# Kernel tuning notes

Measured on AMD Instinct MI355X. Metric: run time of the kernel, lower is better.

## Reference

```python
import jax, jax.numpy as jnp
import numpy as np

EPS = 1e-08

def setup_inputs() -> dict:
    key = jax.random.key(0)
    ks = jax.random.split(key, 5)
    B, T, D, L = 8, 4096, 1024, 24
    data = jax.random.normal(ks[0], (B, T, D), dtype=jnp.float32)
    W_enc = jax.random.normal(ks[1], (L, D), dtype=jnp.float32) * (1.0 / np.sqrt(D))
    b_enc = jax.random.normal(ks[2], (L,), dtype=jnp.float32) * 0.01
    W_dec = jax.random.normal(ks[3], (D, L), dtype=jnp.float32) * (1.0 / np.sqrt(L))
    b_dec = jax.random.normal(ks[4], (D,), dtype=jnp.float32) * 0.01
    ecs = jnp.array([0.1], dtype=jnp.float32)  # error_correction_strength
    ep = jnp.array([1.0], dtype=jnp.float32)   # energy_preservation
    return {"data": data, "W_enc": W_enc, "b_enc": b_enc,
            "W_dec": W_dec, "b_dec": b_dec,
            "error_correction_strength": ecs, "energy_preservation": ep}

def _l2(x):
    return jnp.linalg.norm(x, axis=-1, keepdims=True)

def reference(data, W_enc, b_enc, W_dec, b_dec, error_correction_strength, energy_preservation):
    ecs = error_correction_strength[0]
    ep = energy_preservation[0]
    # --- encode_to_lattice ---
    in_e = _l2(data)                                   # [B,T,1]
    proj = jnp.einsum('btd,ld->btl', data, W_enc) + b_enc
    lattice_points = jnp.round(proj / ecs) * ecs       # quantize to lattice grid
    out_e = _l2(lattice_points)
    lattice = lattice_points * (in_e / (out_e + EPS)) * ep
    # --- decode_from_lattice ---
    in_e2 = _l2(lattice)
    corrected = jnp.where(jnp.abs(lattice) > ecs, lattice, 0.0)
    res = jnp.einsum('btl,dl->btd', corrected, W_dec) + b_dec
    out_e2 = _l2(res)
    return res * (in_e2 / (out_e2 + EPS)) * ep
```

## Files before the change

kernel.cpp:

```cpp
#include <hip/hip_runtime.h>
#include <math.h>

#define EPS 1e-8f

typedef float vfloat4 __attribute__((ext_vector_type(4)));

__global__ void prep_all(const float* __restrict__ W_enc,
                         const float* __restrict__ Wd, const float* __restrict__ bd,
                         float* __restrict__ wt, float* __restrict__ G,
                         float* __restrict__ h, float* __restrict__ bb) {
    int b = blockIdx.x;
    int lane = threadIdx.x;
    if (b < 384) {
        int i = b * 64 + lane;
        int k = i / 24, l = i - k * 24;
        wt[i] = W_enc[l * 1024 + k];
        return;
    }
    b -= 384;
    float s = 0.f;
    if (b < 576) {
        int l = b / 24, m = b - (b / 24) * 24;
        for (int d = lane; d < 1024; d += 64) s = fmaf(Wd[d * 24 + l], Wd[d * 24 + m], s);
    } else if (b < 600) {
        int l = b - 576;
        for (int d = lane; d < 1024; d += 64) s = fmaf(Wd[d * 24 + l], bd[d], s);
    } else {
        for (int d = lane; d < 1024; d += 64) s = fmaf(bd[d], bd[d], s);
    }
    for (int off = 32; off; off >>= 1) s += __shfl_down(s, off);
    if (lane == 0) {
        if (b < 576) G[b] = s;
        else if (b < 600) h[b - 576] = s;
        else *bb = s;
    }
}


constexpr int BROWS   = 128;
constexpr int LD_TILE = 32;
constexpr int TILE_F  = BROWS * LD_TILE;
constexpr int NW      = 8;
constexpr int SMEM_F  = NW * TILE_F;

__global__ __launch_bounds__(512, 2)
void leech_main(const float* __restrict__ data,
                const float* __restrict__ b_enc,
                const float* __restrict__ Wd,
                const float* __restrict__ b_dec,
                const float* __restrict__ ecs_p,
                const float* __restrict__ ep_p,
                const float* __restrict__ wt,
                const float* __restrict__ G,
                const float* __restrict__ h,
                const float* __restrict__ bbp,
                float* __restrict__ out)
{
    __shared__ float smem[SMEM_F];
    const int tid = threadIdx.x;
    const int w = tid >> 6;
    const int r = tid & 63;
    const int rowbase = blockIdx.x * BROWS;

    float* tile = smem + w * TILE_F;

    const int lrow = r >> 3;
    const int lk   = (r & 7) * 4;
    const int rb   = r & 31;

    float proj0[24], proj1[24];
#pragma unroll
    for (int l = 0; l < 24; ++l) { proj0[l] = 0.f; proj1[l] = 0.f; }
    float ssq0 = 0.f, ssq1 = 0.f;

    const int kw = __builtin_amdgcn_readfirstlane((tid >> 6) * 128);

    float4 buf[16];
#pragma unroll
    for (int it = 0; it < 16; ++it)
        buf[it] = *reinterpret_cast<const float4*>(
            data + (size_t)(rowbase + it * 8 + lrow) * 1024 + kw + lk);

    for (int sc = 0; sc < 4; ++sc) {
#pragma unroll
        for (int it = 0; it < 16; ++it) {
            const int row = it * 8 + lrow;
            const int rbw = row & 31;
            float* t = tile + row * LD_TILE;
            t[(lk + 0) ^ rbw] = buf[it].x;
            t[(lk + 1) ^ rbw] = buf[it].y;
            t[(lk + 2) ^ rbw] = buf[it].z;
            t[(lk + 3) ^ rbw] = buf[it].w;
        }
        if (sc < 3) {
            const int k0n = kw + (sc + 1) * 32;
#pragma unroll
            for (int it = 0; it < 16; ++it)
                buf[it] = *reinterpret_cast<const float4*>(
                    data + (size_t)(rowbase + it * 8 + lrow) * 1024 + k0n + lk);
        }
        const float* x0 = tile + r * LD_TILE;
        const float* x1 = tile + (r + 64) * LD_TILE;
        const int kofs = __builtin_amdgcn_readfirstlane(kw + sc * 32);
#pragma unroll 4
        for (int kk = 0; kk < 32; ++kk) {
            const float a = x0[kk ^ rb];
            const float b = x1[kk ^ rb];
            ssq0 = fmaf(a, a, ssq0);
            ssq1 = fmaf(b, b, ssq1);
            const float* wp = wt + (size_t)(kofs + kk) * 24;
#pragma unroll
            for (int l = 0; l < 24; ++l) {
                const float wv = wp[l];
                proj0[l] = fmaf(wv, a, proj0[l]);
                proj1[l] = fmaf(wv, b, proj1[l]);
            }
        }
    }

#pragma unroll
    for (int l = 0; l < 24; ++l) {
        smem[w * TILE_F + l * 64 + r]        = proj0[l];
        smem[w * TILE_F + (24 + l) * 64 + r] = proj1[l];
    }
    smem[w * TILE_F + 48 * 64 + r] = ssq0;
    smem[w * TILE_F + 49 * 64 + r] = ssq1;
    __syncthreads();

    float p0[24], p1[24];
#pragma unroll
    for (int l = 0; l < 24; ++l) {
        float a0 = smem[0 * TILE_F + l * 64 + r] + smem[1 * TILE_F + l * 64 + r];
        float a1 = smem[2 * TILE_F + l * 64 + r] + smem[3 * TILE_F + l * 64 + r];
        float a2 = smem[4 * TILE_F + l * 64 + r] + smem[5 * TILE_F + l * 64 + r];
        float a3 = smem[6 * TILE_F + l * 64 + r] + smem[7 * TILE_F + l * 64 + r];
        p0[l] = (a0 + a1) + (a2 + a3);
        float b0 = smem[0 * TILE_F + (24 + l) * 64 + r] + smem[1 * TILE_F + (24 + l) * 64 + r];
        float b1 = smem[2 * TILE_F + (24 + l) * 64 + r] + smem[3 * TILE_F + (24 + l) * 64 + r];
        float b2 = smem[4 * TILE_F + (24 + l) * 64 + r] + smem[5 * TILE_F + (24 + l) * 64 + r];
        float b3 = smem[6 * TILE_F + (24 + l) * 64 + r] + smem[7 * TILE_F + (24 + l) * 64 + r];
        p1[l] = (b0 + b1) + (b2 + b3);
    }
    float ss0, ss1;
    {
        float a0 = smem[0 * TILE_F + 48 * 64 + r] + smem[1 * TILE_F + 48 * 64 + r];
        float a1 = smem[2 * TILE_F + 48 * 64 + r] + smem[3 * TILE_F + 48 * 64 + r];
        float a2 = smem[4 * TILE_F + 48 * 64 + r] + smem[5 * TILE_F + 48 * 64 + r];
        float a3 = smem[6 * TILE_F + 48 * 64 + r] + smem[7 * TILE_F + 48 * 64 + r];
        ss0 = (a0 + a1) + (a2 + a3);
        float b0 = smem[0 * TILE_F + 49 * 64 + r] + smem[1 * TILE_F + 49 * 64 + r];
        float b1 = smem[2 * TILE_F + 49 * 64 + r] + smem[3 * TILE_F + 49 * 64 + r];
        float b2 = smem[4 * TILE_F + 49 * 64 + r] + smem[5 * TILE_F + 49 * 64 + r];
        float b3 = smem[6 * TILE_F + 49 * 64 + r] + smem[7 * TILE_F + 49 * 64 + r];
        ss1 = (b0 + b1) + (b2 + b3);
    }
    __syncthreads();

    const float ecs = ecs_p[0];
    const float ep  = ep_p[0];

    float c0[24], c1[24];
    float s2a, s2b;
    {
        const float in_e = sqrtf(ss0);
        float lp[24]; float oe = 0.f;
#pragma unroll
        for (int l = 0; l < 24; ++l) {
            const float pp = p0[l] + b_enc[l];
            const float q = rintf(pp / ecs) * ecs;
            lp[l] = q;
            oe = fmaf(q, q, oe);
        }
        const float s1 = in_e / (sqrtf(oe) + EPS) * ep;
        float ie = 0.f;
#pragma unroll
        for (int l = 0; l < 24; ++l) {
            const float lat = lp[l] * s1;
            ie = fmaf(lat, lat, ie);
            c0[l] = (fabsf(lat) > ecs) ? lat : 0.f;
        }
        const float in_e2 = sqrtf(ie);
        float qacc = bbp[0];
#pragma unroll
        for (int l = 0; l < 24; ++l) {
            float s = 2.f * h[l];
#pragma unroll
            for (int m = 0; m < 24; ++m)
                s = fmaf(G[l * 24 + m], c0[m], s);
            qacc = fmaf(s, c0[l], qacc);
        }
        const float out_e2 = sqrtf(fmaxf(qacc, 0.f));
        s2a = in_e2 / (out_e2 + EPS) * ep;
    }
    {
        const float in_e = sqrtf(ss1);
        float lp[24]; float oe = 0.f;
#pragma unroll
        for (int l = 0; l < 24; ++l) {
            const float pp = p1[l] + b_enc[l];
            const float q = rintf(pp / ecs) * ecs;
            lp[l] = q;
            oe = fmaf(q, q, oe);
        }
        const float s1 = in_e / (sqrtf(oe) + EPS) * ep;
        float ie = 0.f;
#pragma unroll
        for (int l = 0; l < 24; ++l) {
            const float lat = lp[l] * s1;
            ie = fmaf(lat, lat, ie);
            c1[l] = (fabsf(lat) > ecs) ? lat : 0.f;
        }
        const float in_e2 = sqrtf(ie);
        float qacc = bbp[0];
#pragma unroll
        for (int l = 0; l < 24; ++l) {
            float s = 2.f * h[l];
#pragma unroll
            for (int m = 0; m < 24; ++m)
                s = fmaf(G[l * 24 + m], c1[m], s);
            qacc = fmaf(s, c1[l], qacc);
        }
        const float out_e2 = sqrtf(fmaxf(qacc, 0.f));
        s2b = in_e2 / (out_e2 + EPS) * ep;
    }

    for (int sc = 0; sc < 4; ++sc) {
        const int d0 = __builtin_amdgcn_readfirstlane(kw + sc * 32);
        float* t0 = tile + r * LD_TILE;
        float* t1 = tile + (r + 64) * LD_TILE;
#pragma unroll 4
        for (int dd = 0; dd < 32; ++dd) {
            const int d = d0 + dd;
            const float* wr = Wd + d * 24;
            const float bv = b_dec[d];
            float acc0 = bv, acc1 = bv;
#pragma unroll
            for (int l = 0; l < 24; ++l) {
                const float wv = wr[l];
                acc0 = fmaf(wv, c0[l], acc0);
                acc1 = fmaf(wv, c1[l], acc1);
            }
            t0[dd ^ rb] = acc0 * s2a;
            t1[dd ^ rb] = acc1 * s2b;
        }
#pragma unroll
        for (int it = 0; it < 16; ++it) {
            const int row = it * 8 + lrow;
            const int rbw = row & 31;
            const float* t = tile + row * LD_TILE;
            vfloat4 v;
            v.x = t[(lk + 0) ^ rbw];
            v.y = t[(lk + 1) ^ rbw];
            v.z = t[(lk + 2) ^ rbw];
            v.w = t[(lk + 3) ^ rbw];
            __builtin_nontemporal_store(v, reinterpret_cast<vfloat4*>(
                out + (size_t)(rowbase + row) * 1024 + d0 + lk));
        }
    }
}


extern "C" void kernel_launch(void* const* d_in, const int* in_sizes, int n_in,
                              void* d_out, int out_size, void* d_ws, size_t ws_size,
                              hipStream_t stream) {
    const float* data  = (const float*)d_in[0];
    const float* W_enc = (const float*)d_in[1];
    const float* b_enc = (const float*)d_in[2];
    const float* W_dec = (const float*)d_in[3];
    const float* b_dec = (const float*)d_in[4];
    const float* ecs   = (const float*)d_in[5];
    const float* ep    = (const float*)d_in[6];
    float* out = (float*)d_out;

    float* ws = (float*)d_ws;
    float* wt = ws;
    float* G  = ws + 24576;
    float* h  = ws + 25152;
    float* bb = ws + 25176;

    const int rows = in_sizes[0] / 1024;

    hipLaunchKernelGGL(prep_all, dim3(985), dim3(64), 0, stream,
                       W_enc, W_dec, b_dec, wt, G, h, bb);
    hipLaunchKernelGGL(leech_main, dim3(rows / BROWS), dim3(512), 0, stream,
                       data, b_enc, W_dec, b_dec, ecs, ep, wt, G, h, bb, out);
}
```

Measured before the change: 312.6 us.

## Load data rows directly into registers and stage weights per-wave in LDS

Removes the swizzled LDS transpose tile for input and output. Each thread now loads its two rows' 32-float chunks straight into vector registers and writes decoder results with direct per-row float4 nontemporal stores. Encoder and decoder weight slices are staged per wave into a small LDS region and read back as float4 broadcasts, with loads for the next chunk issued ahead of compute. The cross-wave reduction buffer now packs both rows as float2. The cost is that lanes access memory 4 KB apart, which may reduce global coalescing efficiency and raise register pressure.

```diff
diff --git a/kernel.cpp b/kernel.cpp
--- a/kernel.cpp
+++ b/kernel.cpp
@@ -4,6 +4,7 @@
 #define EPS 1e-8f
 
 typedef float vfloat4 __attribute__((ext_vector_type(4)));
+typedef float vfloat2 __attribute__((ext_vector_type(2)));
 
 __global__ void prep_all(const float* __restrict__ W_enc,
                          const float* __restrict__ Wd, const float* __restrict__ bd,
@@ -37,11 +38,11 @@
 }
 
 
-constexpr int BROWS   = 128;
-constexpr int LD_TILE = 32;
-constexpr int TILE_F  = BROWS * LD_TILE;
-constexpr int NW      = 8;
-constexpr int SMEM_F  = NW * TILE_F;
+constexpr int BROWS  = 128;
+constexpr int NW     = 8;
+constexpr int WREG_F = 800;
+constexpr int COMB_F = 25 * 64 * 2;
+constexpr int SMEM_F = NW * WREG_F + NW * COMB_F;
 
 __global__ __launch_bounds__(512, 2)
 void leech_main(const float* __restrict__ data,
@@ -62,97 +63,100 @@
     const int r = tid & 63;
     const int rowbase = blockIdx.x * BROWS;
 
-    float* tile = smem + w * TILE_F;
-
-    const int lrow = r >> 3;
-    const int lk   = (r & 7) * 4;
-    const int rb   = r & 31;
+    float* wreg = smem + w * WREG_F;
+    vfloat2* cw = (vfloat2*)(smem + NW * WREG_F) + w * 25 * 64;
+    vfloat2* cb = (vfloat2*)(smem + NW * WREG_F);
+
+    const int kw = __builtin_amdgcn_readfirstlane((tid >> 6) * 128);
+
+    const size_t row0 = (size_t)(rowbase + r);
+    const size_t row1 = row0 + 64;
+    const float* pr0 = data + row0 * 1024 + kw;
+    const float* pr1 = data + row1 * 1024 + kw;
 
     float proj0[24], proj1[24];
 #pragma unroll
     for (int l = 0; l < 24; ++l) { proj0[l] = 0.f; proj1[l] = 0.f; }
     float ssq0 = 0.f, ssq1 = 0.f;
 
-    const int kw = __builtin_amdgcn_readfirstlane((tid >> 6) * 128);
-
-    float4 buf[16];
-#pragma unroll
-    for (int it = 0; it < 16; ++it)
-        buf[it] = *reinterpret_cast<const float4*>(
-            data + (size_t)(rowbase + it * 8 + lrow) * 1024 + kw + lk);
-
-    for (int sc = 0; sc < 4; ++sc) {
-#pragma unroll
-        for (int it = 0; it < 16; ++it) {
-            const int row = it * 8 + lrow;
-            const int rbw = row & 31;
-            float* t = tile + row * LD_TILE;
-            t[(lk + 0) ^ rbw] = buf[it].x;
-            t[(lk + 1) ^ rbw] = buf[it].y;
-            t[(lk + 2) ^ rbw] = buf[it].z;
-            t[(lk + 3) ^ rbw] = buf[it].w;
-        }
-        if (sc < 3) {
-            const int k0n = kw + (sc + 1) * 32;
-#pragma unroll
-            for (int it = 0; it < 16; ++it)
-                buf[it] = *reinterpret_cast<const float4*>(
-                    data + (size_t)(rowbase + it * 8 + lrow) * 1024 + k0n + lk);
-        }
-        const float* x0 = tile + r * LD_TILE;
-        const float* x1 = tile + (r + 64) * LD_TILE;
-        const int kofs = __builtin_amdgcn_readfirstlane(kw + sc * 32);
-#pragma unroll 4
-        for (int kk = 0; kk < 32; ++kk) {
-            const float a = x0[kk ^ rb];
-            const float b = x1[kk ^ rb];
-            ssq0 = fmaf(a, a, ssq0);
-            ssq1 = fmaf(b, b, ssq1);
-            const float* wp = wt + (size_t)(kofs + kk) * 24;
-#pragma unroll
-            for (int l = 0; l < 24; ++l) {
-                const float wv = wp[l];
-                proj0[l] = fmaf(wv, a, proj0[l]);
-                proj1[l] = fmaf(wv, b, proj1[l]);
-            }
-        }
-    }
+    vfloat4 xa0[8], xa1[8], xb0[8], xb1[8];
+    vfloat4 ew0, ew1, ew2;
+
+#define XLOAD(X0, X1, sc) { \
+    _Pragma("unroll") \
+    for (int g = 0; g < 8; ++g) { \
+        X0[g] = *(const vfloat4*)(pr0 + (sc) * 32 + g * 4); \
+        X1[g] = *(const vfloat4*)(pr1 + (sc) * 32 + g * 4); \
+    } }
+
+#define EWLOAD(sc) { \
+    const float* gs_ = wt + (size_t)(kw + (sc) * 32) * 24 + r * 12; \
+    ew0 = *(const vfloat4*)gs_; \
+    ew1 = *(const vfloat4*)(gs_ + 4); \
+    ew2 = *(const vfloat4*)(gs_ + 8); }
+
+#define EWSTORE() { \
+    float* d_ = wreg + r * 12; \
+    *(vfloat4*)d_ = ew0; *(vfloat4*)(d_ + 4) = ew1; *(vfloat4*)(d_ + 8) = ew2; }
+
+#define ENC_COMP(X0, X1) { \
+    _Pragma("unroll") \
+    for (int kk = 0; kk < 32; ++kk) { \
+        const float a = X0[kk >> 2][kk & 3]; \
+        const float b = X1[kk >> 2][kk & 3]; \
+        ssq0 = fmaf(a, a, ssq0); \
+        ssq1 = fmaf(b, b, ssq1); \
+        const float* wr_ = wreg + kk * 24; \
+        vfloat4 q[6]; \
+        _Pragma("unroll") \
+        for (int t = 0; t < 6; ++t) q[t] = *(const vfloat4*)(wr_ + t * 4); \
+        _Pragma("unroll") \
+        for (int l = 0; l < 24; ++l) { \
+            const float wv = q[l >> 2][l & 3]; \
+            proj0[l] = fmaf(wv, a, proj0[l]); \
+            proj1[l] = fmaf(wv, b, proj1[l]); \
+        } \
+    } }
+
+    EWLOAD(0); XLOAD(xa0, xa1, 0); EWSTORE();
+    XLOAD(xb0, xb1, 1); EWLOAD(1);
+    ENC_COMP(xa0, xa1);
+    EWSTORE(); EWLOAD(2); XLOAD(xa0, xa1, 2);
+    ENC_COMP(xb0, xb1);
+    EWSTORE(); EWLOAD(3); XLOAD(xb0, xb1, 3);
+    ENC_COMP(xa0, xa1);
+    EWSTORE();
+    ENC_COMP(xb0, xb1);
 
 #pragma unroll
     for (int l = 0; l < 24; ++l) {
-        smem[w * TILE_F + l * 64 + r]        = proj0[l];
-        smem[w * TILE_F + (24 + l) * 64 + r] = proj1[l];
-    }
-    smem[w * TILE_F + 48 * 64 + r] = ssq0;
-    smem[w * TILE_F + 49 * 64 + r] = ssq1;
+        vfloat2 v; v.x = proj0[l]; v.y = proj1[l];
+        cw[l * 64 + r] = v;
+    }
+    {
+        vfloat2 v; v.x = ssq0; v.y = ssq1;
+        cw[24 * 64 + r] = v;
+    }
     __syncthreads();
 
     float p0[24], p1[24];
 #pragma unroll
     for (int l = 0; l < 24; ++l) {
-        float a0 = smem[0 * TILE_F + l * 64 + r] + smem[1 * TILE_F + l * 64 + r];
-        float a1 = smem[2 * TILE_F + l * 64 + r] + smem[3 * TILE_F + l * 64 + r];
-        float a2 = smem[4 * TILE_F + l * 64 + r] + smem[5 * TILE_F + l * 64 + r];
-        float a3 = smem[6 * TILE_F + l * 64 + r] + smem[7 * TILE_F + l * 64 + r];
-        p0[l] = (a0 + a1) + (a2 + a3);
-        float b0 = smem[0 * TILE_F + (24 + l) * 64 + r] + smem[1 * TILE_F + (24 + l) * 64 + r];
-        float b1 = smem[2 * TILE_F + (24 + l) * 64 + r] + smem[3 * TILE_F + (24 + l) * 64 + r];
-        float b2 = smem[4 * TILE_F + (24 + l) * 64 + r] + smem[5 * TILE_F + (24 + l) * 64 + r];
-        float b3 = smem[6 * TILE_F + (24 + l) * 64 + r] + smem[7 * TILE_F + (24 + l) * 64 + r];
-        p1[l] = (b0 + b1) + (b2 + b3);
+        vfloat2 a0 = cb[(0 * 25 + l) * 64 + r] + cb[(1 * 25 + l) * 64 + r];
+        vfloat2 a1 = cb[(2 * 25 + l) * 64 + r] + cb[(3 * 25 + l) * 64 + r];
+        vfloat2 a2 = cb[(4 * 25 + l) * 64 + r] + cb[(5 * 25 + l) * 64 + r];
+        vfloat2 a3 = cb[(6 * 25 + l) * 64 + r] + cb[(7 * 25 + l) * 64 + r];
+        vfloat2 s = (a0 + a1) + (a2 + a3);
+        p0[l] = s.x; p1[l] = s.y;
     }
     float ss0, ss1;
     {
-        float a0 = smem[0 * TILE_F + 48 * 64 + r] + smem[1 * TILE_F + 48 * 64 + r];
-        float a1 = smem[2 * TILE_F + 48 * 64 + r] + smem[3 * TILE_F + 48 * 64 + r];
-        float a2 = smem[4 * TILE_F + 48 * 64 + r] + smem[5 * TILE_F + 48 * 64 + r];
-        float a3 = smem[6 * TILE_F + 48 * 64 + r] + smem[7 * TILE_F + 48 * 64 + r];
-        ss0 = (a0 + a1) + (a2 + a3);
-        float b0 = smem[0 * TILE_F + 49 * 64 + r] + smem[1 * TILE_F + 49 * 64 + r];
-        float b1 = smem[2 * TILE_F + 49 * 64 + r] + smem[3 * TILE_F + 49 * 64 + r];
-        float b2 = smem[4 * TILE_F + 49 * 64 + r] + smem[5 * TILE_F + 49 * 64 + r];
-        float b3 = smem[6 * TILE_F + 49 * 64 + r] + smem[7 * TILE_F + 49 * 64 + r];
-        ss1 = (b0 + b1) + (b2 + b3);
+        vfloat2 a0 = cb[(0 * 25 + 24) * 64 + r] + cb[(1 * 25 + 24) * 64 + r];
+        vfloat2 a1 = cb[(2 * 25 + 24) * 64 + r] + cb[(3 * 25 + 24) * 64 + r];
+        vfloat2 a2 = cb[(4 * 25 + 24) * 64 + r] + cb[(5 * 25 + 24) * 64 + r];
+        vfloat2 a3 = cb[(6 * 25 + 24) * 64 + r] + cb[(7 * 25 + 24) * 64 + r];
+        vfloat2 s = (a0 + a1) + (a2 + a3);
+        ss0 = s.x; ss1 = s.y;
     }
     __syncthreads();
 
@@ -224,39 +228,65 @@
         s2b = in_e2 / (out_e2 + EPS) * ep;
     }
 
-    for (int sc = 0; sc < 4; ++sc) {
-        const int d0 = __builtin_amdgcn_readfirstlane(kw + sc * 32);
-        float* t0 = tile + r * LD_TILE;
-        float* t1 = tile + (r + 64) * LD_TILE;
-#pragma unroll 4
-        for (int dd = 0; dd < 32; ++dd) {
-            const int d = d0 + dd;
-            const float* wr = Wd + d * 24;
-            const float bv = b_dec[d];
-            float acc0 = bv, acc1 = bv;
-#pragma unroll
-            for (int l = 0; l < 24; ++l) {
-                const float wv = wr[l];
-                acc0 = fmaf(wv, c0[l], acc0);
-                acc1 = fmaf(wv, c1[l], acc1);
-            }
-            t0[dd ^ rb] = acc0 * s2a;
-            t1[dd ^ rb] = acc1 * s2b;
-        }
-#pragma unroll
-        for (int it = 0; it < 16; ++it) {
-            const int row = it * 8 + lrow;
-            const int rbw = row & 31;
-            const float* t = tile + row * LD_TILE;
-            vfloat4 v;
-            v.x = t[(lk + 0) ^ rbw];
-            v.y = t[(lk + 1) ^ rbw];
-            v.z = t[(lk + 2) ^ rbw];
-            v.w = t[(lk + 3) ^ rbw];
-            __builtin_nontemporal_store(v, reinterpret_cast<vfloat4*>(
-                out + (size_t)(rowbase + row) * 1024 + d0 + lk));
-        }
-    }
+    float* po0 = out + row0 * 1024 + kw;
+    float* po1 = out + row1 * 1024 + kw;
+    vfloat4 bld;
+
+#define DWLOAD(sc) { \
+    const float* gs_ = Wd + (size_t)(kw + (sc) * 32) * 24 + r * 12; \
+    ew0 = *(const vfloat4*)gs_; \
+    ew1 = *(const vfloat4*)(gs_ + 4); \
+    ew2 = *(const vfloat4*)(gs_ + 8); \
+    if (r < 8) bld = *(const vfloat4*)(b_dec + kw + (sc) * 32 + r * 4); }
+
+#define DWSTORE() { \
+    float* d_ = wreg + r * 12; \
+    *(vfloat4*)d_ = ew0; *(vfloat4*)(d_ + 4) = ew1; *(vfloat4*)(d_ + 8) = ew2; \
+    if (r < 8) *(vfloat4*)(wreg + 768 + r * 4) = bld; }
+
+#define DEC_COMP(sc) { \
+    _Pragma("unroll") \
+    for (int q8 = 0; q8 < 8; ++q8) { \
+        vfloat4 res0, res1; \
+        _Pragma("unroll") \
+        for (int i = 0; i < 4; ++i) { \
+            const int dd = q8 * 4 + i; \
+            const float* wr_ = wreg + dd * 24; \
+            vfloat4 q[6]; \
+            _Pragma("unroll") \
+            for (int t = 0; t < 6; ++t) q[t] = *(const vfloat4*)(wr_ + t * 4); \
+            const float bv = wreg[768 + dd]; \
+            float acc0 = bv, acc1 = bv; \
+            _Pragma("unroll") \
+            for (int l = 0; l < 24; ++l) { \
+                const float wv = q[l >> 2][l & 3]; \
+                acc0 = fmaf(wv, c0[l], acc0); \
+                acc1 = fmaf(wv, c1[l], acc1); \
+            } \
+            res0[i] = acc0 * s2a; \
+            res1[i] = acc1 * s2b; \
+        } \
+        __builtin_nontemporal_store(res0, (vfloat4*)(po0 + (sc) * 32 + q8 * 4)); \
+        __builtin_nontemporal_store(res1, (vfloat4*)(po1 + (sc) * 32 + q8 * 4)); \
+    } }
+
+    DWLOAD(0); DWSTORE();
+    DWLOAD(1);
+    DEC_COMP(0);
+    DWSTORE(); DWLOAD(2);
+    DEC_COMP(1);
+    DWSTORE(); DWLOAD(3);
+    DEC_COMP(2);
+    DWSTORE();
+    DEC_COMP(3);
+
+#undef XLOAD
+#undef EWLOAD
+#undef EWSTORE
+#undef ENC_COMP
+#undef DWLOAD
+#undef DWSTORE
+#undef DEC_COMP
 }
 
 
```

Result: slower. 806.3 us (+157.9%).
